# Kernel tuning notes

Hardware: AMD Instinct MI355X
Metric: run time of the kernel (lower is better)

The kernel has to match this reference:

```python
import jax, jax.numpy as jnp
import numpy as np

B = 8192
D1 = 1024
D2 = 1024
H = 4096  # subnet hidden width
SCALE_LIMIT = 1.0


def _mlp(x, W1, b1, W2, b2):
    # Linear -> ReLU -> Linear
    return jnp.maximum(x @ W1 + b1, 0.0) @ W2 + b2


def setup_inputs() -> dict:
    key = jax.random.key(0)
    ks = jax.random.split(key, 17)
    inp = {"x": jax.random.normal(ks[0], (B, D1 + D2), dtype=jnp.float32)}
    # four subnets: s1,t1 map d2->d1 ; s2,t2 map d1->d2
    specs = {"s1": (D2, D1), "t1": (D2, D1), "s2": (D1, D2), "t2": (D1, D2)}
    i = 1
    for name, (din, dout) in specs.items():
        inp[f"{name}_W1"] = 0.02 * jax.random.normal(ks[i], (din, H), dtype=jnp.float32); i += 1
        inp[f"{name}_b1"] = jnp.zeros((H,), dtype=jnp.float32)
        inp[f"{name}_W2"] = 0.02 * jax.random.normal(ks[i], (H, dout), dtype=jnp.float32); i += 1
        inp[f"{name}_b2"] = jnp.zeros((dout,), dtype=jnp.float32)
    return inp


def reference(x,
              s1_W1, s1_b1, s1_W2, s1_b2,
              t1_W1, t1_b1, t1_W2, t1_b2,
              s2_W1, s2_b1, s2_W2, s2_b2,
              t2_W1, t2_b1, t2_W2, t2_b2):
    x1, x2 = x[:, :D1], x[:, D1:]
    # first half-step: update x1 conditioned on x2
    s2v = jnp.tanh(_mlp(x2, s1_W1, s1_b1, s1_W2, s1_b2)) * SCALE_LIMIT  # [B, D1]
    t2v = _mlp(x2, t1_W1, t1_b1, t1_W2, t1_b2)                          # [B, D1]
    y1 = x1 * jnp.exp(s2v) + t2v
    # second half-step: update x2 conditioned on y1
    s1v = jnp.tanh(_mlp(y1, s2_W1, s2_b1, s2_W2, s2_b2)) * SCALE_LIMIT  # [B, D2]
    t1v = _mlp(y1, t2_W1, t2_b1, t2_W2, t2_b2)                          # [B, D2]
    y2 = x2 * jnp.exp(s1v) + t1v
    y = jnp.concatenate([y1, y2], axis=1)  # [B, D1+D2]
    # exact triangular-coupling log-det (what the autograd loop computes per-sample)
    log_det = jnp.sum(s2v, axis=1) + jnp.sum(s1v, axis=1)  # [B]
    return y, log_det
```

## Files before the change

### kernel.cpp

```cpp
#include <hip/hip_runtime.h>
#include <hip/hip_bf16.h>
#include <cstdint>
#include <cstddef>

#define BDIM 8192
#define D1 1024
#define HDIM 4096

#define BM 128
#define BN 128
#define BK 64

typedef __attribute__((ext_vector_type(8))) short short8;
typedef __attribute__((ext_vector_type(4))) float f32x4;

__device__ inline void async_load16(const void* g, void* l) {
  __builtin_amdgcn_global_load_lds(
      (const __attribute__((address_space(1))) void*)g,
      (__attribute__((address_space(3))) void*)l,
      16 , 0 , 0 );
}

__device__ inline unsigned short f2bf(float f) {
  union { float f; uint32_t u; } v; v.f = f;
  uint32_t u = v.u;
  uint32_t r = u + 0x7FFFu + ((u >> 16) & 1u);
  return (unsigned short)(r >> 16);
}

__global__ __launch_bounds__(256, 2)
void gemm1_fused(const unsigned short* __restrict__ A,
                 const unsigned short* __restrict__ Bs,
                 const unsigned short* __restrict__ Bt,
                 const float* __restrict__ bias_s,
                 const float* __restrict__ bias_t,
                 unsigned short* __restrict__ Cs,
                 unsigned short* __restrict__ Ct) {
  const int K = 1024, N = 4096;
  __shared__ __align__(16) unsigned short lsA[BM * BK];
  __shared__ __align__(16) unsigned short lsS[BN * BK];
  __shared__ __align__(16) unsigned short lsT[BN * BK];

  const int tid  = threadIdx.x;
  const int wave = tid >> 6;
  const int lane = tid & 63;
  const int quad = lane >> 4;
  const int l15  = lane & 15;
  const int m0 = blockIdx.y * BM;
  const int n0 = blockIdx.x * BN;
  const int wrow = (wave >> 1) * 64;
  const int wcol = (wave & 1) * 64;

  f32x4 accS[4][4] = {};
  f32x4 accT[4][4] = {};

  for (int k0 = 0; k0 < K; k0 += BK) {
    __syncthreads();
#pragma unroll
    for (int i = 0; i < 4; ++i) {
      int s   = (wave * 4 + i) * 64 + lane;
      int row = s >> 3;
      int kg  = (s & 7) ^ (row & 7);
      async_load16(A  + (long)(m0 + row) * K + k0 + kg * 8, &lsA[(wave * 4 + i) * 512]);
      async_load16(Bs + (long)(n0 + row) * K + k0 + kg * 8, &lsS[(wave * 4 + i) * 512]);
      async_load16(Bt + (long)(n0 + row) * K + k0 + kg * 8, &lsT[(wave * 4 + i) * 512]);
    }
    __syncthreads();

#pragma unroll
    for (int ks = 0; ks < 2; ++ks) {
      short8 af[4], bs[4], bt[4];
      const int kg = ks * 4 + quad;
#pragma unroll
      for (int t = 0; t < 4; ++t) {
        int row = wrow + t * 16 + l15;
        af[t] = *(const short8*)&lsA[(row * 8 + (kg ^ (row & 7))) * 8];
        int col = wcol + t * 16 + l15;
        int pb  = col * 8 + (kg ^ (col & 7));
        bs[t] = *(const short8*)&lsS[pb * 8];
        bt[t] = *(const short8*)&lsT[pb * 8];
      }
#pragma unroll
      for (int mt = 0; mt < 4; ++mt)
#pragma unroll
        for (int nt = 0; nt < 4; ++nt) {
          accS[mt][nt] = __builtin_amdgcn_mfma_f32_16x16x32_bf16(
              af[mt], bs[nt], accS[mt][nt], 0, 0, 0);
          accT[mt][nt] = __builtin_amdgcn_mfma_f32_16x16x32_bf16(
              af[mt], bt[nt], accT[mt][nt], 0, 0, 0);
        }
    }
  }

#pragma unroll
  for (int nt = 0; nt < 4; ++nt) {
    int col = n0 + wcol + nt * 16 + l15;
    float bvs = bias_s[col], bvt = bias_t[col];
#pragma unroll
    for (int mt = 0; mt < 4; ++mt)
#pragma unroll
      for (int r = 0; r < 4; ++r) {
        long row = m0 + wrow + mt * 16 + quad * 4 + r;
        float vs = accS[mt][nt][r] + bvs;
        float vt = accT[mt][nt][r] + bvt;
        Cs[row * N + col] = f2bf(vs > 0.f ? vs : 0.f);
        Ct[row * N + col] = f2bf(vt > 0.f ? vt : 0.f);
      }
  }
}

__global__ __launch_bounds__(256, 2)
void gemm2_fused(const unsigned short* __restrict__ As,
                 const unsigned short* __restrict__ At,
                 const unsigned short* __restrict__ Bs,
                 const unsigned short* __restrict__ Bt,
                 const float* __restrict__ bias_s,
                 const float* __restrict__ bias_t,
                 const float* __restrict__ x,
                 float* __restrict__ y_out,
                 unsigned short* __restrict__ y_bf,
                 float* __restrict__ ld_out,
                 int moff, int stage) {
  const int K = 4096;
  __shared__ __align__(16) unsigned short lsAs[BM * BK];
  __shared__ __align__(16) unsigned short lsAt[BM * BK];
  __shared__ __align__(16) unsigned short lsS[BN * BK];
  __shared__ __align__(16) unsigned short lsT[BN * BK];
  __shared__ float rowsum[BM];

  const int tid  = threadIdx.x;
  const int wave = tid >> 6;
  const int lane = tid & 63;
  const int quad = lane >> 4;
  const int l15  = lane & 15;
  const int m0 = blockIdx.y * BM;
  const int n0 = blockIdx.x * BN;
  const int wrow = (wave >> 1) * 64;
  const int wcol = (wave & 1) * 64;

  f32x4 accS[4][4] = {};
  f32x4 accT[4][4] = {};

  for (int k0 = 0; k0 < K; k0 += BK) {
    __syncthreads();
#pragma unroll
    for (int i = 0; i < 4; ++i) {
      int s   = (wave * 4 + i) * 64 + lane;
      int row = s >> 3;
      int kg  = (s & 7) ^ (row & 7);
      long go = (long)row * K + k0 + kg * 8;
      async_load16(As + (long)m0 * K + go, &lsAs[(wave * 4 + i) * 512]);
      async_load16(At + (long)m0 * K + go, &lsAt[(wave * 4 + i) * 512]);
      async_load16(Bs + (long)n0 * K + go, &lsS[(wave * 4 + i) * 512]);
      async_load16(Bt + (long)n0 * K + go, &lsT[(wave * 4 + i) * 512]);
    }
    __syncthreads();

#pragma unroll
    for (int ks = 0; ks < 2; ++ks) {
      short8 as[4], at[4], bs[4], bt[4];
      const int kg = ks * 4 + quad;
#pragma unroll
      for (int t = 0; t < 4; ++t) {
        int row = wrow + t * 16 + l15;
        int pa  = row * 8 + (kg ^ (row & 7));
        as[t] = *(const short8*)&lsAs[pa * 8];
        at[t] = *(const short8*)&lsAt[pa * 8];
        int col = wcol + t * 16 + l15;
        int pb  = col * 8 + (kg ^ (col & 7));
        bs[t] = *(const short8*)&lsS[pb * 8];
        bt[t] = *(const short8*)&lsT[pb * 8];
      }
#pragma unroll
      for (int mt = 0; mt < 4; ++mt)
#pragma unroll
        for (int nt = 0; nt < 4; ++nt) {
          accS[mt][nt] = __builtin_amdgcn_mfma_f32_16x16x32_bf16(
              as[mt], bs[nt], accS[mt][nt], 0, 0, 0);
          accT[mt][nt] = __builtin_amdgcn_mfma_f32_16x16x32_bf16(
              at[mt], bt[nt], accT[mt][nt], 0, 0, 0);
        }
    }
  }

  if (tid < BM) rowsum[tid] = 0.f;
  __syncthreads();

  const int off = stage ? D1 : 0;
  float bvs[4], bvt[4];
#pragma unroll
  for (int nt = 0; nt < 4; ++nt) {
    int col = n0 + wcol + nt * 16 + l15;
    bvs[nt] = bias_s[col];
    bvt[nt] = bias_t[col];
  }
#pragma unroll
  for (int mt = 0; mt < 4; ++mt)
#pragma unroll
    for (int r = 0; r < 4; ++r) {
      long grow = (long)moff + m0 + wrow + mt * 16 + quad * 4 + r;
      float rs = 0.f;
#pragma unroll
      for (int nt = 0; nt < 4; ++nt) {
        int col = n0 + wcol + nt * 16 + l15;
        float sv = tanhf(accS[mt][nt][r] + bvs[nt]);
        rs += sv;
        float t  = accT[mt][nt][r] + bvt[nt];
        float y  = x[grow * (2 * D1) + off + col] * __expf(sv) + t;
        y_out[grow * (2 * D1) + off + col] = y;
        if (y_bf) y_bf[grow * D1 + col] = f2bf(y);
      }
#pragma unroll
      for (int o = 8; o > 0; o >>= 1) rs += __shfl_down(rs, o, 16);
      if (l15 == 0) atomicAdd(&rowsum[wrow + mt * 16 + quad * 4 + r], rs);
    }
  __syncthreads();
  if (tid < BM) atomicAdd(&ld_out[moff + m0 + tid], rowsum[tid]);
}

__global__ __launch_bounds__(256)
void transpose_cast(const float* __restrict__ in, unsigned short* __restrict__ out,
                    int R, int C) {
  __shared__ float tile[32][33];
  const int bx = blockIdx.x * 32;
  const int by = blockIdx.y * 32;
  const int tx = threadIdx.x & 31;
  const int ty = threadIdx.x >> 5;
  for (int j = ty; j < 32; j += 8)
    tile[j][tx] = in[(long)(by + j) * C + bx + tx];
  __syncthreads();
  for (int j = ty; j < 32; j += 8)
    out[(long)(bx + j) * R + by + tx] = f2bf(tile[tx][j]);
}

__global__ __launch_bounds__(256)
void cast_x2(const float* __restrict__ x, unsigned short* __restrict__ x2b) {
  long i = (long)blockIdx.x * 256 + threadIdx.x;
  long row = i >> 10, col = i & 1023;
  x2b[i] = f2bf(x[row * (2 * D1) + D1 + col]);
}

__global__ __launch_bounds__(256)
void zero_f(float* __restrict__ p, int n) {
  int i = blockIdx.x * 256 + threadIdx.x;
  if (i < n) p[i] = 0.f;
}

extern "C" void kernel_launch(void* const* d_in, const int* in_sizes, int n_in,
                              void* d_out, int out_size, void* d_ws, size_t ws_size,
                              hipStream_t stream) {
  const float* x     = (const float*)d_in[0];
  const float* s1_W1 = (const float*)d_in[1];
  const float* s1_b1 = (const float*)d_in[2];
  const float* s1_W2 = (const float*)d_in[3];
  const float* s1_b2 = (const float*)d_in[4];
  const float* t1_W1 = (const float*)d_in[5];
  const float* t1_b1 = (const float*)d_in[6];
  const float* t1_W2 = (const float*)d_in[7];
  const float* t1_b2 = (const float*)d_in[8];
  const float* s2_W1 = (const float*)d_in[9];
  const float* s2_b1 = (const float*)d_in[10];
  const float* s2_W2 = (const float*)d_in[11];
  const float* s2_b2 = (const float*)d_in[12];
  const float* t2_W1 = (const float*)d_in[13];
  const float* t2_b1 = (const float*)d_in[14];
  const float* t2_W2 = (const float*)d_in[15];
  const float* t2_b2 = (const float*)d_in[16];

  const size_t MB = 1024UL * 1024UL;
  int NC = 32;
  {
    const int cand[6] = {1, 2, 4, 8, 16, 32};
    for (int i = 0; i < 6; ++i) {
      size_t need = 80 * MB + (128 * MB) / (size_t)cand[i];
      if (need <= ws_size) { NC = cand[i]; break; }
    }
  }
  const int Mrows = BDIM / NC;

  char* ws = (char*)d_ws;
  unsigned short* w1t[4], * w2t[4];
  for (int i = 0; i < 4; ++i) {
    w1t[i] = (unsigned short*)(ws + (8 * (size_t)i) * MB);
    w2t[i] = (unsigned short*)(ws + (32 + 8 * (size_t)i) * MB);
  }
  unsigned short* xyb = (unsigned short*)(ws + 64 * MB);
  size_t hbytes = (size_t)Mrows * HDIM * 2;
  unsigned short* h_s = (unsigned short*)(ws + 80 * MB);
  unsigned short* h_t = (unsigned short*)(ws + 80 * MB + hbytes);

  float* y_out  = (float*)d_out;
  float* ld_out = (float*)d_out + (long)BDIM * (2 * D1);

  zero_f<<<(BDIM + 255) / 256, 256, 0, stream>>>(ld_out, BDIM);
  cast_x2<<<(BDIM * D1) / 256, 256, 0, stream>>>(x, xyb);
  transpose_cast<<<dim3(HDIM / 32, D1 / 32), 256, 0, stream>>>(s1_W1, w1t[0], D1, HDIM);
  transpose_cast<<<dim3(HDIM / 32, D1 / 32), 256, 0, stream>>>(t1_W1, w1t[1], D1, HDIM);
  transpose_cast<<<dim3(HDIM / 32, D1 / 32), 256, 0, stream>>>(s2_W1, w1t[2], D1, HDIM);
  transpose_cast<<<dim3(HDIM / 32, D1 / 32), 256, 0, stream>>>(t2_W1, w1t[3], D1, HDIM);
  transpose_cast<<<dim3(D1 / 32, HDIM / 32), 256, 0, stream>>>(s1_W2, w2t[0], HDIM, D1);
  transpose_cast<<<dim3(D1 / 32, HDIM / 32), 256, 0, stream>>>(t1_W2, w2t[1], HDIM, D1);
  transpose_cast<<<dim3(D1 / 32, HDIM / 32), 256, 0, stream>>>(s2_W2, w2t[2], HDIM, D1);
  transpose_cast<<<dim3(D1 / 32, HDIM / 32), 256, 0, stream>>>(t2_W2, w2t[3], HDIM, D1);

  for (int c = 0; c < NC; ++c) {
    const int moff = c * Mrows;
    unsigned short* xA = xyb + (size_t)moff * D1;

    gemm1_fused<<<dim3(HDIM / BN, Mrows / BM), 256, 0, stream>>>(
        xA, w1t[0], w1t[1], s1_b1, t1_b1, h_s, h_t);
    gemm2_fused<<<dim3(D1 / BN, Mrows / BM), 256, 0, stream>>>(
        h_s, h_t, w2t[0], w2t[1], s1_b2, t1_b2, x, y_out, xyb, ld_out, moff, 0);

    gemm1_fused<<<dim3(HDIM / BN, Mrows / BM), 256, 0, stream>>>(
        xA, w1t[2], w1t[3], s2_b1, t2_b1, h_s, h_t);
    gemm2_fused<<<dim3(D1 / BN, Mrows / BM), 256, 0, stream>>>(
        h_s, h_t, w2t[2], w2t[3], s2_b2, t2_b2, x, y_out, nullptr, ld_out, moff, 1);
  }
}
```

Before: 916.0 us.

## Replace fused GEMMs with pipelined 256x256 GEMM plus separate coupling kernel

Replaces the two 128x128 fused GEMM kernels with one generic 256x256-tile, 512-thread GEMM. It double-buffers LDS with async global-to-LDS loads, partial vmcnt waits, setprio around the MFMA blocks, XCD-aware tile remapping and LDS-staged vectorised stores. The tanh/exp coupling and log-det row sum move into a separate row-wise kernel that reads bf16 s/t outputs, so atomics and the zero-init kernel go away. When the workspace is large enough, the whole batch runs in one pass with s/t merged via z-grid and weight transposes reused. This costs an extra bf16 round trip for s and t through global memory and lower precision of pre-activation outputs.

New measurement: 833.8 us. 9.0% less time.

```diff
diff --git a/kernel.cpp b/kernel.cpp
--- a/kernel.cpp
+++ b/kernel.cpp
@@ -1,5 +1,4 @@
 #include <hip/hip_runtime.h>
-#include <hip/hip_bf16.h>
 #include <cstdint>
 #include <cstddef>
 
@@ -7,12 +6,9 @@
 #define D1 1024
 #define HDIM 4096
 
-#define BM 128
-#define BN 128
-#define BK 64
-
 typedef __attribute__((ext_vector_type(8))) short short8;
 typedef __attribute__((ext_vector_type(4))) float f32x4;
+typedef __attribute__((ext_vector_type(4))) unsigned short u16x4;
 
 __device__ inline void async_load16(const void* g, void* l) {
   __builtin_amdgcn_global_load_lds(
@@ -27,195 +23,209 @@
   uint32_t r = u + 0x7FFFu + ((u >> 16) & 1u);
   return (unsigned short)(r >> 16);
 }
-
-__global__ __launch_bounds__(256, 2)
-void gemm1_fused(const unsigned short* __restrict__ A,
-                 const unsigned short* __restrict__ Bs,
-                 const unsigned short* __restrict__ Bt,
-                 const float* __restrict__ bias_s,
-                 const float* __restrict__ bias_t,
-                 unsigned short* __restrict__ Cs,
-                 unsigned short* __restrict__ Ct) {
-  const int K = 1024, N = 4096;
-  __shared__ __align__(16) unsigned short lsA[BM * BK];
-  __shared__ __align__(16) unsigned short lsS[BN * BK];
-  __shared__ __align__(16) unsigned short lsT[BN * BK];
+__device__ inline float bf2f(unsigned short u) {
+  union { uint32_t u; float f; } v; v.u = (uint32_t)u << 16; return v.f;
+}
+
+__global__ __launch_bounds__(512, 2)
+void gemm8(const unsigned short* __restrict__ A0,
+           const unsigned short* __restrict__ A1, int lda,
+           const unsigned short* __restrict__ B0,
+           const unsigned short* __restrict__ B1,
+           const float* __restrict__ bias0, const float* __restrict__ bias1,
+           unsigned short* __restrict__ C0, unsigned short* __restrict__ C1,
+           int ldc, int K, int relu) {
+  __shared__ __align__(16) unsigned short smem[65536];
+
+  const int z = blockIdx.z;
+  const unsigned short* A  = z ? A1 : A0;
+  const unsigned short* Bw = z ? B1 : B0;
+  const float* biasP       = z ? bias1 : bias0;
+  unsigned short* C        = z ? C1 : C0;
+
+  const int nX  = gridDim.x;
+  const int nwg = gridDim.x * gridDim.y;
+  const int bid = blockIdx.y * gridDim.x + blockIdx.x;
+  const int q = nwg >> 3, r = nwg & 7;
+  const int xcd = bid & 7, rest = bid >> 3;
+  const int wg = (xcd < r ? xcd * (q + 1) : r * (q + 1) + (xcd - r) * q) + rest;
+  const int tm = wg / nX, tn = wg % nX;
+  const int m0 = tm * 256, n0 = tn * 256;
 
   const int tid  = threadIdx.x;
-  const int wave = tid >> 6;
-  const int lane = tid & 63;
-  const int quad = lane >> 4;
-  const int l15  = lane & 15;
-  const int m0 = blockIdx.y * BM;
-  const int n0 = blockIdx.x * BN;
-  const int wrow = (wave >> 1) * 64;
-  const int wcol = (wave & 1) * 64;
-
-  f32x4 accS[4][4] = {};
-  f32x4 accT[4][4] = {};
-
-  for (int k0 = 0; k0 < K; k0 += BK) {
-    __syncthreads();
-#pragma unroll
-    for (int i = 0; i < 4; ++i) {
-      int s   = (wave * 4 + i) * 64 + lane;
-      int row = s >> 3;
-      int kg  = (s & 7) ^ (row & 7);
-      async_load16(A  + (long)(m0 + row) * K + k0 + kg * 8, &lsA[(wave * 4 + i) * 512]);
-      async_load16(Bs + (long)(n0 + row) * K + k0 + kg * 8, &lsS[(wave * 4 + i) * 512]);
-      async_load16(Bt + (long)(n0 + row) * K + k0 + kg * 8, &lsT[(wave * 4 + i) * 512]);
+  const int wave = tid >> 6, lane = tid & 63;
+  const int quad = lane >> 4, l15 = lane & 15;
+  const int wm = wave >> 2, wn = wave & 3;
+
+  const int sr    = tid >> 2;
+  const int sslot = (tid & 3) ^ ((tid >> 3) & 3);
+  const unsigned short* gA = A  + (long)(m0 + sr) * lda + sslot * 8;
+  const unsigned short* gB = Bw + (long)(n0 + sr) * K   + sslot * 8;
+
+  const int swz = ((quad ^ ((l15 >> 1) & 3)) << 3);
+  const unsigned short* aB = smem + wm * 4096  + l15 * 32 + swz;
+  const unsigned short* bB = smem + 32768 + wn * 2048 + l15 * 32 + swz;
+
+  f32x4 acc[8][4] = {};
+  const int NT = K >> 6;
+
+#define STAGE_A(NB, SL, KT) { \
+  unsigned short* lw = smem + (NB)*16384 + (SL)*8192 + wave*512; \
+  const unsigned short* g = gA + (long)(KT)*64 + (SL)*32; \
+  async_load16(g, lw); \
+  async_load16(g + 128*(long)lda, lw + 4096); }
+
+#define STAGE_B(NB, SL, KT) { \
+  unsigned short* lw = smem + 32768 + (NB)*16384 + (SL)*8192 + wave*512; \
+  const unsigned short* g = gB + (long)(KT)*64 + (SL)*32; \
+  async_load16(g, lw); \
+  async_load16(g + 128*(long)K, lw + 4096); }
+
+#define READ_A(dst, BUF, SL, MH) { \
+  const unsigned short* p = aB + (BUF)*16384 + (SL)*8192 + (MH)*2048; \
+  dst[0] = *(const short8*)(p);        dst[1] = *(const short8*)(p + 512); \
+  dst[2] = *(const short8*)(p + 1024); dst[3] = *(const short8*)(p + 1536); }
+
+#define READ_B(dst, BUF, SL) { \
+  const unsigned short* p = bB + (BUF)*16384 + (SL)*8192; \
+  dst[0] = *(const short8*)(p);        dst[1] = *(const short8*)(p + 512); \
+  dst[2] = *(const short8*)(p + 1024); dst[3] = *(const short8*)(p + 1536); }
+
+#define MFMA16(MH, AV, BV) \
+  _Pragma("unroll") \
+  for (int mt = 0; mt < 4; ++mt) { \
+    _Pragma("unroll") \
+    for (int nt = 0; nt < 4; ++nt) { \
+      acc[(MH)*4 + mt][nt] = __builtin_amdgcn_mfma_f32_16x16x32_bf16( \
+          AV[mt], BV[nt], acc[(MH)*4 + mt][nt], 0, 0, 0); \
+    } }
+
+#define BARRIER() asm volatile("s_barrier" ::: "memory")
+#define VMCNT4()  asm volatile("s_waitcnt vmcnt(4)" ::: "memory")
+
+#define TILE_BODY(BUF, NB, TNX) { \
+  short8 a0[4], a1[4], b0v[4], b1v[4]; \
+   \
+  READ_A(a0, BUF, 0, 0); READ_B(b0v, BUF, 0); \
+  STAGE_A(NB, 0, TNX); \
+  BARRIER(); \
+  __builtin_amdgcn_s_setprio(1); MFMA16(0, a0, b0v); __builtin_amdgcn_s_setprio(0); \
+  BARRIER(); \
+   \
+  READ_A(a1, BUF, 0, 1); \
+  STAGE_B(NB, 0, TNX); \
+  VMCNT4(); \
+  BARRIER(); \
+  __builtin_amdgcn_s_setprio(1); MFMA16(1, a1, b0v); __builtin_amdgcn_s_setprio(0); \
+  BARRIER(); \
+   \
+  READ_A(a0, BUF, 1, 0); READ_B(b1v, BUF, 1); \
+  STAGE_A(NB, 1, TNX); \
+  BARRIER(); \
+  __builtin_amdgcn_s_setprio(1); MFMA16(0, a0, b1v); __builtin_amdgcn_s_setprio(0); \
+  BARRIER(); \
+   \
+  READ_A(a1, BUF, 1, 1); \
+  STAGE_B(NB, 1, TNX); \
+  VMCNT4(); \
+  BARRIER(); \
+  __builtin_amdgcn_s_setprio(1); MFMA16(1, a1, b1v); __builtin_amdgcn_s_setprio(0); \
+  BARRIER(); \
+}
+
+  STAGE_A(0, 0, 0); STAGE_B(0, 0, 0); STAGE_A(0, 1, 0); STAGE_B(0, 1, 0);
+  VMCNT4();
+  BARRIER();
+
+#pragma unroll 1
+  for (int t = 0; t < NT; t += 2) {
+    const int tnx1 = t + 1;
+    const int tnx2 = (t + 2 < NT) ? t + 2 : NT - 1;
+    TILE_BODY(0, 1, tnx1);
+    TILE_BODY(1, 0, tnx2);
+  }
+
+  asm volatile("s_waitcnt vmcnt(0)" ::: "memory");
+  BARRIER();
+
+  unsigned short* sc = smem + wave * 8192;
+#pragma unroll
+  for (int nt = 0; nt < 4; ++nt) {
+    const int col = n0 + wn * 64 + nt * 16 + l15;
+    const float bv = biasP[col];
+#pragma unroll
+    for (int mt = 0; mt < 8; ++mt) {
+#pragma unroll
+      for (int rr = 0; rr < 4; ++rr) {
+        const int lrow = mt * 16 + quad * 4 + rr;
+        float v = acc[mt][nt][rr] + bv;
+        if (relu) v = v > 0.f ? v : 0.f;
+        sc[lrow * 64 + ((nt * 16 + l15) ^ (((lrow >> 2) & 3) << 4))] = f2bf(v);
+      }
     }
-    __syncthreads();
-
-#pragma unroll
-    for (int ks = 0; ks < 2; ++ks) {
-      short8 af[4], bs[4], bt[4];
-      const int kg = ks * 4 + quad;
-#pragma unroll
-      for (int t = 0; t < 4; ++t) {
-        int row = wrow + t * 16 + l15;
-        af[t] = *(const short8*)&lsA[(row * 8 + (kg ^ (row & 7))) * 8];
-        int col = wcol + t * 16 + l15;
-        int pb  = col * 8 + (kg ^ (col & 7));
-        bs[t] = *(const short8*)&lsS[pb * 8];
-        bt[t] = *(const short8*)&lsT[pb * 8];
-      }
-#pragma unroll
-      for (int mt = 0; mt < 4; ++mt)
-#pragma unroll
-        for (int nt = 0; nt < 4; ++nt) {
-          accS[mt][nt] = __builtin_amdgcn_mfma_f32_16x16x32_bf16(
-              af[mt], bs[nt], accS[mt][nt], 0, 0, 0);
-          accT[mt][nt] = __builtin_amdgcn_mfma_f32_16x16x32_bf16(
-              af[mt], bt[nt], accT[mt][nt], 0, 0, 0);
-        }
-    }
-  }
-
-#pragma unroll
-  for (int nt = 0; nt < 4; ++nt) {
-    int col = n0 + wcol + nt * 16 + l15;
-    float bvs = bias_s[col], bvt = bias_t[col];
-#pragma unroll
-    for (int mt = 0; mt < 4; ++mt)
-#pragma unroll
-      for (int r = 0; r < 4; ++r) {
-        long row = m0 + wrow + mt * 16 + quad * 4 + r;
-        float vs = accS[mt][nt][r] + bvs;
-        float vt = accT[mt][nt][r] + bvt;
-        Cs[row * N + col] = f2bf(vs > 0.f ? vs : 0.f);
-        Ct[row * N + col] = f2bf(vt > 0.f ? vt : 0.f);
-      }
-  }
-}
-
-__global__ __launch_bounds__(256, 2)
-void gemm2_fused(const unsigned short* __restrict__ As,
-                 const unsigned short* __restrict__ At,
-                 const unsigned short* __restrict__ Bs,
-                 const unsigned short* __restrict__ Bt,
-                 const float* __restrict__ bias_s,
-                 const float* __restrict__ bias_t,
-                 const float* __restrict__ x,
-                 float* __restrict__ y_out,
-                 unsigned short* __restrict__ y_bf,
-                 float* __restrict__ ld_out,
-                 int moff, int stage) {
-  const int K = 4096;
-  __shared__ __align__(16) unsigned short lsAs[BM * BK];
-  __shared__ __align__(16) unsigned short lsAt[BM * BK];
-  __shared__ __align__(16) unsigned short lsS[BN * BK];
-  __shared__ __align__(16) unsigned short lsT[BN * BK];
-  __shared__ float rowsum[BM];
-
-  const int tid  = threadIdx.x;
-  const int wave = tid >> 6;
-  const int lane = tid & 63;
-  const int quad = lane >> 4;
-  const int l15  = lane & 15;
-  const int m0 = blockIdx.y * BM;
-  const int n0 = blockIdx.x * BN;
-  const int wrow = (wave >> 1) * 64;
-  const int wcol = (wave & 1) * 64;
-
-  f32x4 accS[4][4] = {};
-  f32x4 accT[4][4] = {};
-
-  for (int k0 = 0; k0 < K; k0 += BK) {
-    __syncthreads();
-#pragma unroll
-    for (int i = 0; i < 4; ++i) {
-      int s   = (wave * 4 + i) * 64 + lane;
-      int row = s >> 3;
-      int kg  = (s & 7) ^ (row & 7);
-      long go = (long)row * K + k0 + kg * 8;
-      async_load16(As + (long)m0 * K + go, &lsAs[(wave * 4 + i) * 512]);
-      async_load16(At + (long)m0 * K + go, &lsAt[(wave * 4 + i) * 512]);
-      async_load16(Bs + (long)n0 * K + go, &lsS[(wave * 4 + i) * 512]);
-      async_load16(Bt + (long)n0 * K + go, &lsT[(wave * 4 + i) * 512]);
-    }
-    __syncthreads();
-
-#pragma unroll
-    for (int ks = 0; ks < 2; ++ks) {
-      short8 as[4], at[4], bs[4], bt[4];
-      const int kg = ks * 4 + quad;
-#pragma unroll
-      for (int t = 0; t < 4; ++t) {
-        int row = wrow + t * 16 + l15;
-        int pa  = row * 8 + (kg ^ (row & 7));
-        as[t] = *(const short8*)&lsAs[pa * 8];
-        at[t] = *(const short8*)&lsAt[pa * 8];
-        int col = wcol + t * 16 + l15;
-        int pb  = col * 8 + (kg ^ (col & 7));
-        bs[t] = *(const short8*)&lsS[pb * 8];
-        bt[t] = *(const short8*)&lsT[pb * 8];
-      }
-#pragma unroll
-      for (int mt = 0; mt < 4; ++mt)
-#pragma unroll
-        for (int nt = 0; nt < 4; ++nt) {
-          accS[mt][nt] = __builtin_amdgcn_mfma_f32_16x16x32_bf16(
-              as[mt], bs[nt], accS[mt][nt], 0, 0, 0);
-          accT[mt][nt] = __builtin_amdgcn_mfma_f32_16x16x32_bf16(
-              at[mt], bt[nt], accT[mt][nt], 0, 0, 0);
-        }
-    }
-  }
-
-  if (tid < BM) rowsum[tid] = 0.f;
+  }
+  const long rowbase = m0 + wm * 128;
+  const int colbase  = n0 + wn * 64;
+#pragma unroll
+  for (int i = 0; i < 16; ++i) {
+    const int L   = i * 1024 + lane * 16;
+    const int row = L >> 7;
+    const int sp  = (L & 127) >> 4;
+    const int cg  = sp ^ ((((row) >> 2) & 3) << 1);
+    short8 v = *(const short8*)&sc[row * 64 + sp * 8];
+    *(short8*)&C[(rowbase + row) * (long)ldc + colbase + cg * 8] = v;
+  }
+
+#undef STAGE_A
+#undef STAGE_B
+#undef READ_A
+#undef READ_B
+#undef MFMA16
+#undef BARRIER
+#undef VMCNT4
+#undef TILE_BODY
+}
+
+__global__ __launch_bounds__(256)
+void couple(const unsigned short* sb, const unsigned short* __restrict__ tb,
+            const float* __restrict__ x, float* __restrict__ y,
+            unsigned short* y1b, float* __restrict__ ld,
+            long growoff, int xoff, int addld) {
+  __shared__ float wsum[4];
+  const int row = blockIdx.x;
+  const long grow = growoff + row;
+  const int c = threadIdx.x * 4;
+
+  u16x4 sv4 = *(const u16x4*)&sb[(long)row * 1024 + c];
+  u16x4 tv4 = *(const u16x4*)&tb[(long)row * 1024 + c];
+  f32x4 xv  = *(const f32x4*)&x[grow * 2048 + xoff + c];
+  f32x4 yv;
+  unsigned short yb[4];
+  float rs = 0.f;
+#pragma unroll
+  for (int j = 0; j < 4; ++j) {
+    float s  = bf2f(sv4[j]);
+    float t  = bf2f(tv4[j]);
+    float sv = tanhf(s);
+    rs += sv;
+    float yy = xv[j] * __expf(sv) + t;
+    yv[j] = yy;
+    yb[j] = f2bf(yy);
+  }
+  *(f32x4*)&y[grow * 2048 + xoff + c] = yv;
+  if (y1b) {
+    u16x4 o; o[0] = yb[0]; o[1] = yb[1]; o[2] = yb[2]; o[3] = yb[3];
+    *(u16x4*)&y1b[(long)row * 1024 + c] = o;
+  }
+#pragma unroll
+  for (int o = 32; o > 0; o >>= 1) rs += __shfl_down(rs, o);
+  const int wv = threadIdx.x >> 6, ln = threadIdx.x & 63;
+  if (ln == 0) wsum[wv] = rs;
   __syncthreads();
-
-  const int off = stage ? D1 : 0;
-  float bvs[4], bvt[4];
-#pragma unroll
-  for (int nt = 0; nt < 4; ++nt) {
-    int col = n0 + wcol + nt * 16 + l15;
-    bvs[nt] = bias_s[col];
-    bvt[nt] = bias_t[col];
-  }
-#pragma unroll
-  for (int mt = 0; mt < 4; ++mt)
-#pragma unroll
-    for (int r = 0; r < 4; ++r) {
-      long grow = (long)moff + m0 + wrow + mt * 16 + quad * 4 + r;
-      float rs = 0.f;
-#pragma unroll
-      for (int nt = 0; nt < 4; ++nt) {
-        int col = n0 + wcol + nt * 16 + l15;
-        float sv = tanhf(accS[mt][nt][r] + bvs[nt]);
-        rs += sv;
-        float t  = accT[mt][nt][r] + bvt[nt];
-        float y  = x[grow * (2 * D1) + off + col] * __expf(sv) + t;
-        y_out[grow * (2 * D1) + off + col] = y;
-        if (y_bf) y_bf[grow * D1 + col] = f2bf(y);
-      }
-#pragma unroll
-      for (int o = 8; o > 0; o >>= 1) rs += __shfl_down(rs, o, 16);
-      if (l15 == 0) atomicAdd(&rowsum[wrow + mt * 16 + quad * 4 + r], rs);
-    }
-  __syncthreads();
-  if (tid < BM) atomicAdd(&ld_out[moff + m0 + tid], rowsum[tid]);
+  if (threadIdx.x == 0) {
+    float tot = wsum[0] + wsum[1] + wsum[2] + wsum[3];
+    if (addld) ld[grow] += tot; else ld[grow] = tot;
+  }
 }
 
 __global__ __launch_bounds__(256)
@@ -238,12 +248,6 @@
   long i = (long)blockIdx.x * 256 + threadIdx.x;
   long row = i >> 10, col = i & 1023;
   x2b[i] = f2bf(x[row * (2 * D1) + D1 + col]);
-}
-
-__global__ __launch_bounds__(256)
-void zero_f(float* __restrict__ p, int n) {
-  int i = blockIdx.x * 256 + threadIdx.x;
-  if (i < n) p[i] = 0.f;
 }
 
 extern "C" void kernel_launch(void* const* d_in, const int* in_sizes, int n_in,
@@ -268,53 +272,83 @@
   const float* t2_b2 = (const float*)d_in[16];
 
   const size_t MB = 1024UL * 1024UL;
-  int NC = 32;
-  {
-    const int cand[6] = {1, 2, 4, 8, 16, 32};
-    for (int i = 0; i < 6; ++i) {
-      size_t need = 80 * MB + (128 * MB) / (size_t)cand[i];
-      if (need <= ws_size) { NC = cand[i]; break; }
-    }
-  }
-  const int Mrows = BDIM / NC;
-
-  char* ws = (char*)d_ws;
-  unsigned short* w1t[4], * w2t[4];
-  for (int i = 0; i < 4; ++i) {
-    w1t[i] = (unsigned short*)(ws + (8 * (size_t)i) * MB);
-    w2t[i] = (unsigned short*)(ws + (32 + 8 * (size_t)i) * MB);
-  }
-  unsigned short* xyb = (unsigned short*)(ws + 64 * MB);
-  size_t hbytes = (size_t)Mrows * HDIM * 2;
-  unsigned short* h_s = (unsigned short*)(ws + 80 * MB);
-  unsigned short* h_t = (unsigned short*)(ws + 80 * MB + hbytes);
-
   float* y_out  = (float*)d_out;
   float* ld_out = (float*)d_out + (long)BDIM * (2 * D1);
-
-  zero_f<<<(BDIM + 255) / 256, 256, 0, stream>>>(ld_out, BDIM);
-  cast_x2<<<(BDIM * D1) / 256, 256, 0, stream>>>(x, xyb);
-  transpose_cast<<<dim3(HDIM / 32, D1 / 32), 256, 0, stream>>>(s1_W1, w1t[0], D1, HDIM);
-  transpose_cast<<<dim3(HDIM / 32, D1 / 32), 256, 0, stream>>>(t1_W1, w1t[1], D1, HDIM);
-  transpose_cast<<<dim3(HDIM / 32, D1 / 32), 256, 0, stream>>>(s2_W1, w1t[2], D1, HDIM);
-  transpose_cast<<<dim3(HDIM / 32, D1 / 32), 256, 0, stream>>>(t2_W1, w1t[3], D1, HDIM);
-  transpose_cast<<<dim3(D1 / 32, HDIM / 32), 256, 0, stream>>>(s1_W2, w2t[0], HDIM, D1);
-  transpose_cast<<<dim3(D1 / 32, HDIM / 32), 256, 0, stream>>>(t1_W2, w2t[1], HDIM, D1);
-  transpose_cast<<<dim3(D1 / 32, HDIM / 32), 256, 0, stream>>>(s2_W2, w2t[2], HDIM, D1);
-  transpose_cast<<<dim3(D1 / 32, HDIM / 32), 256, 0, stream>>>(t2_W2, w2t[3], HDIM, D1);
-
-  for (int c = 0; c < NC; ++c) {
-    const int moff = c * Mrows;
-    unsigned short* xA = xyb + (size_t)moff * D1;
-
-    gemm1_fused<<<dim3(HDIM / BN, Mrows / BM), 256, 0, stream>>>(
-        xA, w1t[0], w1t[1], s1_b1, t1_b1, h_s, h_t);
-    gemm2_fused<<<dim3(D1 / BN, Mrows / BM), 256, 0, stream>>>(
-        h_s, h_t, w2t[0], w2t[1], s1_b2, t1_b2, x, y_out, xyb, ld_out, moff, 0);
-
-    gemm1_fused<<<dim3(HDIM / BN, Mrows / BM), 256, 0, stream>>>(
-        xA, w1t[2], w1t[3], s2_b1, t2_b1, h_s, h_t);
-    gemm2_fused<<<dim3(D1 / BN, Mrows / BM), 256, 0, stream>>>(
-        h_s, h_t, w2t[2], w2t[3], s2_b2, t2_b2, x, y_out, nullptr, ld_out, moff, 1);
-  }
-}
+  char* ws = (char*)d_ws;
+
+  if (ws_size >= 192 * MB) {
+    unsigned short* w1a = (unsigned short*)(ws + 0 * MB);
+    unsigned short* w1b = (unsigned short*)(ws + 8 * MB);
+    unsigned short* w2a = (unsigned short*)(ws + 16 * MB);
+    unsigned short* w2b = (unsigned short*)(ws + 24 * MB);
+    unsigned short* x2b = (unsigned short*)(ws + 32 * MB);
+    unsigned short* tb  = (unsigned short*)(ws + 48 * MB);
+    unsigned short* h   = (unsigned short*)(ws + 64 * MB);
+
+    cast_x2<<<(BDIM * D1) / 256, 256, 0, stream>>>(x, x2b);
+    transpose_cast<<<dim3(HDIM / 32, D1 / 32), 256, 0, stream>>>(s1_W1, w1a, D1, HDIM);
+    transpose_cast<<<dim3(HDIM / 32, D1 / 32), 256, 0, stream>>>(t1_W1, w1b, D1, HDIM);
+    transpose_cast<<<dim3(D1 / 32, HDIM / 32), 256, 0, stream>>>(s1_W2, w2a, HDIM, D1);
+    transpose_cast<<<dim3(D1 / 32, HDIM / 32), 256, 0, stream>>>(t1_W2, w2b, HDIM, D1);
+
+    gemm8<<<dim3(16, 32, 2), 512, 0, stream>>>(x2b, x2b, D1, w1a, w1b,
+        s1_b1, t1_b1, h, h + 4096, 2 * HDIM, D1, 1);
+    transpose_cast<<<dim3(HDIM / 32, D1 / 32), 256, 0, stream>>>(s2_W1, w1a, D1, HDIM);
+    transpose_cast<<<dim3(HDIM / 32, D1 / 32), 256, 0, stream>>>(t2_W1, w1b, D1, HDIM);
+    gemm8<<<dim3(4, 32, 2), 512, 0, stream>>>(h, h + 4096, 2 * HDIM, w2a, w2b,
+        s1_b2, t1_b2, x2b , tb, D1, HDIM, 0);
+    transpose_cast<<<dim3(D1 / 32, HDIM / 32), 256, 0, stream>>>(s2_W2, w2a, HDIM, D1);
+    transpose_cast<<<dim3(D1 / 32, HDIM / 32), 256, 0, stream>>>(t2_W2, w2b, HDIM, D1);
+    couple<<<BDIM, 256, 0, stream>>>(x2b, tb, x, y_out, x2b ,
+                                     ld_out, 0, 0, 0);
+    gemm8<<<dim3(16, 32, 2), 512, 0, stream>>>(x2b, x2b, D1, w1a, w1b,
+        s2_b1, t2_b1, h, h + 4096, 2 * HDIM, D1, 1);
+    gemm8<<<dim3(4, 32, 2), 512, 0, stream>>>(h, h + 4096, 2 * HDIM, w2a, w2b,
+        s2_b2, t2_b2, x2b , tb, D1, HDIM, 0);
+    couple<<<BDIM, 256, 0, stream>>>(x2b, tb, x, y_out, nullptr, ld_out, 0, D1, 1);
+  } else {
+    int NC = 2;
+    while (NC < 16) {
+      size_t need = 80 * MB + (16 * MB) / NC + (128 * MB) / NC;
+      if (need <= ws_size) break;
+      NC <<= 1;
+    }
+    const int Mrows = BDIM / NC;
+    unsigned short* w1s1 = (unsigned short*)(ws + 0 * MB);
+    unsigned short* w1t1 = (unsigned short*)(ws + 8 * MB);
+    unsigned short* w1s2 = (unsigned short*)(ws + 16 * MB);
+    unsigned short* w1t2 = (unsigned short*)(ws + 24 * MB);
+    unsigned short* w2s1 = (unsigned short*)(ws + 32 * MB);
+    unsigned short* w2t1 = (unsigned short*)(ws + 40 * MB);
+    unsigned short* w2s2 = (unsigned short*)(ws + 48 * MB);
+    unsigned short* w2t2 = (unsigned short*)(ws + 56 * MB);
+    unsigned short* x2b  = (unsigned short*)(ws + 64 * MB);
+    unsigned short* tb   = (unsigned short*)(ws + 80 * MB);
+    unsigned short* h    = (unsigned short*)(ws + 80 * MB + (16 * MB) / NC);
+
+    cast_x2<<<(BDIM * D1) / 256, 256, 0, stream>>>(x, x2b);
+    transpose_cast<<<dim3(HDIM / 32, D1 / 32), 256, 0, stream>>>(s1_W1, w1s1, D1, HDIM);
+    transpose_cast<<<dim3(HDIM / 32, D1 / 32), 256, 0, stream>>>(t1_W1, w1t1, D1, HDIM);
+    transpose_cast<<<dim3(HDIM / 32, D1 / 32), 256, 0, stream>>>(s2_W1, w1s2, D1, HDIM);
+    transpose_cast<<<dim3(HDIM / 32, D1 / 32), 256, 0, stream>>>(t2_W1, w1t2, D1, HDIM);
+    transpose_cast<<<dim3(D1 / 32, HDIM / 32), 256, 0, stream>>>(s1_W2, w2s1, HDIM, D1);
+    transpose_cast<<<dim3(D1 / 32, HDIM / 32), 256, 0, stream>>>(t1_W2, w2t1, HDIM, D1);
+    transpose_cast<<<dim3(D1 / 32, HDIM / 32), 256, 0, stream>>>(s2_W2, w2s2, HDIM, D1);
+    transpose_cast<<<dim3(D1 / 32, HDIM / 32), 256, 0, stream>>>(t2_W2, w2t2, HDIM, D1);
+
+    for (int c = 0; c < NC; ++c) {
+      const long moff = (long)c * Mrows;
+      unsigned short* xA = x2b + moff * D1;
+      gemm8<<<dim3(16, Mrows / 256, 2), 512, 0, stream>>>(xA, xA, D1, w1s1, w1t1,
+          s1_b1, t1_b1, h, h + 4096, 2 * HDIM, D1, 1);
+      gemm8<<<dim3(4, Mrows / 256, 2), 512, 0, stream>>>(h, h + 4096, 2 * HDIM,
+          w2s1, w2t1, s1_b2, t1_b2, xA, tb, D1, HDIM, 0);
+      couple<<<Mrows, 256, 0, stream>>>(xA, tb, x, y_out, xA, ld_out, moff, 0, 0);
+      gemm8<<<dim3(16, Mrows / 256, 2), 512, 0, stream>>>(xA, xA, D1, w1s2, w1t2,
+          s2_b1, t2_b1, h, h + 4096, 2 * HDIM, D1, 1);
+      gemm8<<<dim3(4, Mrows / 256, 2), 512, 0, stream>>>(h, h + 4096, 2 * HDIM,
+          w2s2, w2t2, s2_b2, t2_b2, xA, tb, D1, HDIM, 0);
+      couple<<<Mrows, 256, 0, stream>>>(xA, tb, x, y_out, nullptr, ld_out, moff, D1, 1);
+    }
+  }
+}
```
